# Performance work log

Hardware: AMD Instinct MI355X
Metric: run time of the kernel (lower is better)

The kernel has to match this reference:

```python
import jax, jax.numpy as jnp
import numpy as np

NUM_CLIP_VIT_FEAT = 576  # default kwarg of mixed_mask


def _mixed_mask(pad_ends, full_starts, full_ends, bt2i, blm, B, S):
    # Faithful translation of OmniAttentionMechanism.mixed_mask evaluated over
    # all (b, q_idx, kv_idx). Note python operator precedence: & binds tighter
    # than ^, so the original expression is (A&t2i) ^ (B&C&lm) ^ (D&mmu).
    q_idx = jnp.arange(S)[:, None]          # [S,1]
    kv_idx = jnp.arange(S)[None, :]         # [1,S]
    causal_qk = q_idx >= kv_idx             # [S,S]
    # kv_idx < pad_ends[b, kv_idx]  ->  arange(S) < pad_ends  (per batch row)
    pad_region = jnp.arange(S) < pad_ends   # [B,S] over kv
    causal = (~pad_region)[:, None, :] & causal_qk[None]              # [B,S,S]
    # full block: kv in [full_starts[q], full_ends[q])
    full = (kv_idx < full_ends[:, None]) & (kv_idx >= full_starts[:, None])  # [S,S]
    eye = q_idx == kv_idx                                             # [S,S]
    t2i = eye[None] ^ (causal | full[None])                           # [B,S,S]
    lm = causal_qk                                                    # [S,S]
    mmu = causal_qk | (kv_idx <= NUM_CLIP_VIT_FEAT + 3)               # [S,S]
    b = jnp.arange(B)[:, None, None]
    mask = ((b < bt2i) & t2i) \
         ^ ((b >= bt2i) & (b < bt2i + blm) & lm[None]) \
         ^ ((b >= bt2i + blm) & mmu[None])
    return mask  # [B,S,S] bool


def setup_inputs() -> dict:
    key = jax.random.key(0)
    B_T2I, B_LM, B_MMU = 4, 4, 4
    B, H, S, D = B_T2I + B_LM + B_MMU, 8, 1024, 64
    k1, k2, k3 = jax.random.split(key, 3)
    q = jax.random.normal(k1, (B, H, S, D), jnp.float32)
    k = jax.random.normal(k2, (B, H, S, D), jnp.float32)
    v = jax.random.normal(k3, (B, H, S, D), jnp.float32)

    # full_starts/full_ends from image_begin_ends=[(512,1024)]
    full_starts = np.arange(S)
    full_ends = np.arange(S)
    for ib, ie in [(512, 1024)]:
        full_starts[ib:ie] = ib
        full_ends[ib:ie] = ie

    # pad_ends from default pad_begin_ends=[(0,256),(0,300),(0,400),(0,0)]
    pad_ends = np.tile(np.arange(S), (B, 1))
    for cnt, (pb, pe) in enumerate([(0, 256), (0, 300), (0, 400), (0, 0)]):
        pad_ends[cnt, pb:pe] = pe

    return {
        "q": q, "k": k, "v": v,
        "pad_ends": jnp.asarray(pad_ends, jnp.int32),
        "full_starts": jnp.asarray(full_starts, jnp.int32),
        "full_ends": jnp.asarray(full_ends, jnp.int32),
        "batch_size_t2i": B_T2I,
        "batch_size_lm": B_LM,
    }


def reference(q, k, v, pad_ends, full_starts, full_ends, batch_size_t2i, batch_size_lm):
    B, H, S, D = q.shape
    mask = _mixed_mask(pad_ends, full_starts, full_ends,
                       batch_size_t2i, batch_size_lm, B, S)      # [B,S,S]
    scale = 1.0 / jnp.sqrt(jnp.asarray(D, q.dtype))
    scores = jnp.einsum('bhqd,bhkd->bhqk', q, k) * scale          # [B,H,S,S]
    scores = jnp.where(mask[:, None], scores, jnp.asarray(-1e30, scores.dtype))
    attn = jax.nn.softmax(scores, axis=-1)
    return jnp.einsum('bhqk,bhkd->bhqd', attn, v)
```

## Files before the change

### kernel.cpp

```cpp
#include <hip/hip_runtime.h>


typedef __attribute__((ext_vector_type(8))) short short8;
typedef __attribute__((ext_vector_type(4))) float floatx4;

#define S_LEN 1024
#define D_DIM 64
#define H_NUM 8
#define B_NUM 12
#define BT2I_CONST 4
#define BLM_CONST 4
#define NUM_CLIP_P3 579
#define KV_ELEMS (B_NUM * H_NUM * S_LEN * D_DIM)
#define P_EPS 7.888609052210118e-31f

__device__ __forceinline__ float bf2f(short s) {
    unsigned int u = ((unsigned int)(unsigned short)s) << 16;
    return __builtin_bit_cast(float, u);
}
__device__ __forceinline__ short f2bf(float f) {
    unsigned int u = __builtin_bit_cast(unsigned int, f);
    unsigned int r = (u + 0x7fffu + ((u >> 16) & 1u)) >> 16;
    return (short)(unsigned short)r;
}
__device__ __forceinline__ short scale_bf(short x) {
    float f = bf2f(x) * 0.125f;
    return (short)(unsigned short)(__builtin_bit_cast(unsigned int, f) >> 16);
}
__device__ __forceinline__ int detect_bf16(const unsigned int* q) {
    int l = threadIdx.x & 63;
    unsigned int w = q[l];
    unsigned int e = (w >> 7) & 0xffu;
    bool sane = (e >= 100u && e <= 140u);
    unsigned long long m = __ballot(sane);
    return (__popcll(m) > 32) ? 1 : 0;
}

__global__ __launch_bounds__(256)
void preprocess_kv(const void* __restrict__ Kv, const void* __restrict__ Vv,
                   const unsigned int* __restrict__ Qw,
                   short* __restrict__ Kw, short* __restrict__ Vtw) {
    __shared__ short Ls[64][66];
    const int is_bf16 = detect_bf16(Qw);
    const int x = blockIdx.x;
    const int t = threadIdx.x;
    if (x < 3072) {
        long long i0 = ((long long)x * 256 + t) * 8;
        short8 out;
        if (is_bf16) {
            out = *(const short8*)((const short*)Kv + i0);
        } else {
            const floatx4* p = (const floatx4*)((const float*)Kv + i0);
            floatx4 f0 = p[0], f1 = p[1];
            #pragma unroll
            for (int j = 0; j < 4; ++j) { out[j] = f2bf(f0[j]); out[4 + j] = f2bf(f1[j]); }
        }
        *(short8*)(Kw + i0) = out;
    } else {
        const int idx = x - 3072;
        const int tile = idx & 15, bh = idx >> 4;
        const int kvbase = tile * 64;
        const long long base = (long long)bh * S_LEN * D_DIM;
        #pragma unroll
        for (int j = 0; j < 4; ++j) {
            int lin = j * 1024 + t * 4;
            int row = lin >> 6, col = lin & 63;
            long long src = base + (long long)(kvbase + row) * D_DIM + col;
            if (is_bf16) {
                const short* p = (const short*)Vv + src;
                Ls[row][col] = p[0]; Ls[row][col + 1] = p[1];
                Ls[row][col + 2] = p[2]; Ls[row][col + 3] = p[3];
            } else {
                floatx4 f = *(const floatx4*)((const float*)Vv + src);
                Ls[row][col] = f2bf(f[0]); Ls[row][col + 1] = f2bf(f[1]);
                Ls[row][col + 2] = f2bf(f[2]); Ls[row][col + 3] = f2bf(f[3]);
            }
        }
        __syncthreads();
        const int d = t >> 2, k0 = (t & 3) * 16;
        short tmp[16];
        #pragma unroll
        for (int j = 0; j < 16; ++j) tmp[j] = Ls[k0 + j][d];
        long long dst = (long long)bh * D_DIM * S_LEN + (long long)d * S_LEN + kvbase + k0;
        *(short8*)(Vtw + dst)     = *(short8*)&tmp[0];
        *(short8*)(Vtw + dst + 8) = *(short8*)&tmp[8];
    }
}

__global__ __launch_bounds__(256, 3)
void omni_attn_main(const void* __restrict__ Qv, const int* __restrict__ pad_ends,
                    const int* __restrict__ fstarts, const int* __restrict__ fends,
                    const short* __restrict__ Kw, const short* __restrict__ Vtw,
                    float* __restrict__ Out) {
    __shared__ short Ks[64][72];
    __shared__ short Vts[64][72];
    __shared__ short Ps[4][32][72];
    __shared__ unsigned int padbits[32];

    const int lid = blockIdx.x;
    const int h = lid & 7;
    const int perm = lid >> 3;
    const int b = perm >> 3;
    const int j = perm & 7;
    const int lpt[8] = {7, 0, 6, 1, 5, 2, 4, 3};
    const int qtb = lpt[j];
    const int qb0 = qtb * 128;

    const int t = threadIdx.x;
    const int wq = t >> 6;
    const int l = t & 63;
    const int lane16 = l & 15;
    const int quad = l >> 4;

    const int is_bf16 = detect_bf16((const unsigned int*)Qv);
    const int cls = (b < BT2I_CONST) ? 0 : ((b < BT2I_CONST + BLM_CONST) ? 1 : 2);
    const int bh = b * H_NUM + h;
    const long long base = (long long)bh * S_LEN * D_DIM;

    #pragma unroll
    for (int kk = 0; kk < 4; ++kk) {
        int k = kk * 256 + t;
        bool nonpad = (k >= pad_ends[b * S_LEN + k]);
        unsigned long long m = __ballot(nonpad);
        if (l == 0) {
            int widx = kk * 8 + wq * 2;
            padbits[widx]     = (unsigned int)m;
            padbits[widx + 1] = (unsigned int)(m >> 32);
        }
    }
    __syncthreads();

    int fs_min, fe_max, fnp;
    {
        int fsv = min(fstarts[qb0 + l], fstarts[qb0 + 64 + l]);
        int fev = max(fends[qb0 + l],   fends[qb0 + 64 + l]);
        unsigned int word = 0u;
        if (l < 32) word = padbits[l];
        int pos = word ? (l * 32 + __builtin_ctz(word)) : 0x7fffffff;
        #pragma unroll
        for (int off = 1; off < 64; off <<= 1) {
            fsv = min(fsv, __shfl_xor(fsv, off, 64));
            fev = max(fev, __shfl_xor(fev, off, 64));
            pos = min(pos, __shfl_xor(pos, off, 64));
        }
        fs_min = fsv; fe_max = fev; fnp = pos;
    }
    const int qmax_blk = qb0 + 127;
    const bool risky = (cls == 0) && (fnp >= qb0) && (fnp <= qmax_blk);

    short8 aq[2][2];
    #pragma unroll
    for (int rb = 0; rb < 2; ++rb) {
        const int row = qb0 + wq * 32 + rb * 16 + lane16;
        if (is_bf16) {
            const short8* qp = (const short8*)((const short*)Qv + base
                                               + (long long)row * D_DIM + quad * 8);
            short8 r0 = qp[0], r1 = qp[4];
            #pragma unroll
            for (int jj = 0; jj < 8; ++jj) {
                aq[rb][0][jj] = scale_bf(r0[jj]);
                aq[rb][1][jj] = scale_bf(r1[jj]);
            }
        } else {
            const floatx4* qp = (const floatx4*)((const float*)Qv + base
                                                 + (long long)row * D_DIM + quad * 8);
            floatx4 f0 = qp[0], f1 = qp[1], f2 = qp[8], f3 = qp[9];
            #pragma unroll
            for (int jj = 0; jj < 4; ++jj) {
                aq[rb][0][jj]     = f2bf(f0[jj] * 0.125f);
                aq[rb][0][4 + jj] = f2bf(f1[jj] * 0.125f);
                aq[rb][1][jj]     = f2bf(f2[jj] * 0.125f);
                aq[rb][1][4 + jj] = f2bf(f3[jj] * 0.125f);
            }
        }
    }

    int qg[2][4], fs[2][4], fe[2][4];
    #pragma unroll
    for (int rb = 0; rb < 2; ++rb)
        #pragma unroll
        for (int r = 0; r < 4; ++r) {
            qg[rb][r] = qb0 + wq * 32 + rb * 16 + quad * 4 + r;
            fs[rb][r] = fstarts[qg[rb][r]];
            fe[rb][r] = fends[qg[rb][r]];
        }

    floatx4 Oc[2][4];
    float lsum[2][4];
    #pragma unroll
    for (int rb = 0; rb < 2; ++rb) {
        #pragma unroll
        for (int c = 0; c < 4; ++c) Oc[rb][c] = (floatx4){0.f, 0.f, 0.f, 0.f};
        #pragma unroll
        for (int r = 0; r < 4; ++r) lsum[rb][r] = 0.f;
    }

    const short* Kbh  = Kw  + base;
    const short* Vtbh = Vtw + (long long)bh * D_DIM * S_LEN;

    for (int kt = 0; kt < 16; ++kt) {
        const int kvbase = kt * 64;
        const unsigned int w0 = padbits[kt * 2], w1 = padbits[kt * 2 + 1];
        bool keep;
        if (cls == 0) {
            bool allpad = (w0 | w1) == 0u;
            keep = risky ||
                   ((kvbase < fe_max) && (kvbase + 64 > fs_min)) ||
                   ((kvbase <= qmax_blk) && (!allpad || (kvbase >= qb0)));
        } else if (cls == 1) {
            keep = (kvbase <= qmax_blk);
        } else {
            keep = (kvbase <= qmax_blk) || (kvbase <= NUM_CLIP_P3);
        }
        if (!keep) continue;

        __syncthreads();

        {
            const int r0 = t >> 2, s = t & 3;
            const short8* gk = (const short8*)(Kbh + (long long)(kvbase + r0) * D_DIM);
            *(short8*)&Ks[r0][s * 8]       = gk[s];
            *(short8*)&Ks[r0][(s + 4) * 8] = gk[s + 4];
            const short8* gv = (const short8*)(Vtbh + (long long)r0 * S_LEN + kvbase);
            *(short8*)&Vts[r0][s * 8]       = gv[s];
            *(short8*)&Vts[r0][(s + 4) * 8] = gv[s + 4];
        }
        __syncthreads();

        int col[4], knp[4];
        #pragma unroll
        for (int f = 0; f < 4; ++f) {
            int c16 = f * 16 + lane16;
            col[f] = kvbase + c16;
            knp[f] = (int)(((f < 2 ? w0 : w1) >> (c16 & 31)) & 1u);
        }

        #pragma unroll
        for (int rb = 0; rb < 2; ++rb) {
            floatx4 sc[4];
            #pragma unroll
            for (int f = 0; f < 4; ++f) {
                short8 b0 = *(const short8*)&Ks[f * 16 + lane16][quad * 8];
                short8 b1 = *(const short8*)&Ks[f * 16 + lane16][32 + quad * 8];
                floatx4 c = (floatx4){0.f, 0.f, 0.f, 0.f};
                c = __builtin_amdgcn_mfma_f32_16x16x32_bf16(aq[rb][0], b0, c, 0, 0, 0);
                c = __builtin_amdgcn_mfma_f32_16x16x32_bf16(aq[rb][1], b1, c, 0, 0, 0);
                sc[f] = c;
            }
            if (cls == 0) {
                #pragma unroll
                for (int r = 0; r < 4; ++r) {
                    const int q = qg[rb][r];
                    #pragma unroll
                    for (int f = 0; f < 4; ++f) {
                        const int k = col[f];
                        bool causal = knp[f] && (q >= k);
                        bool full   = (k >= fs[rb][r]) && (k < fe[rb][r]);
                        bool m      = (q == k) != (causal || full);
                        sc[f][r] = m ? sc[f][r] : -1e30f;
                    }
                }
            } else if (cls == 1) {
                #pragma unroll
                for (int r = 0; r < 4; ++r) {
                    const int q = qg[rb][r];
                    #pragma unroll
                    for (int f = 0; f < 4; ++f)
                        sc[f][r] = (q >= col[f]) ? sc[f][r] : -1e30f;
                }
            } else {
                #pragma unroll
                for (int r = 0; r < 4; ++r) {
                    const int q = qg[rb][r];
                    #pragma unroll
                    for (int f = 0; f < 4; ++f) {
                        bool m = (q >= col[f]) || (col[f] <= NUM_CLIP_P3);
                        sc[f][r] = m ? sc[f][r] : -1e30f;
                    }
                }
            }
            #pragma unroll
            for (int r = 0; r < 4; ++r) {
                #pragma unroll
                for (int f = 0; f < 4; ++f) {
                    float p = __expf(sc[f][r]) + P_EPS;
                    sc[f][r] = p;
                    lsum[rb][r] += p;
                }
            }
            #pragma unroll
            for (int r = 0; r < 4; ++r)
                #pragma unroll
                for (int f = 0; f < 4; ++f)
                    Ps[wq][rb * 16 + quad * 4 + r][f * 16 + lane16] = f2bf(sc[f][r]);
        }

        asm volatile("s_waitcnt lgkmcnt(0)" ::: "memory");

        short8 pa[2][2];
        #pragma unroll
        for (int rb = 0; rb < 2; ++rb) {
            pa[rb][0] = *(const short8*)&Ps[wq][rb * 16 + lane16][quad * 8];
            pa[rb][1] = *(const short8*)&Ps[wq][rb * 16 + lane16][32 + quad * 8];
        }
        #pragma unroll
        for (int c = 0; c < 4; ++c) {
            short8 b0 = *(const short8*)&Vts[c * 16 + lane16][quad * 8];
            short8 b1 = *(const short8*)&Vts[c * 16 + lane16][32 + quad * 8];
            Oc[0][c] = __builtin_amdgcn_mfma_f32_16x16x32_bf16(pa[0][0], b0, Oc[0][c], 0, 0, 0);
            Oc[0][c] = __builtin_amdgcn_mfma_f32_16x16x32_bf16(pa[0][1], b1, Oc[0][c], 0, 0, 0);
            Oc[1][c] = __builtin_amdgcn_mfma_f32_16x16x32_bf16(pa[1][0], b0, Oc[1][c], 0, 0, 0);
            Oc[1][c] = __builtin_amdgcn_mfma_f32_16x16x32_bf16(pa[1][1], b1, Oc[1][c], 0, 0, 0);
        }
    }

    #pragma unroll
    for (int rb = 0; rb < 2; ++rb) {
        float* ob = Out + ((long long)bh * S_LEN + qb0 + wq * 32 + rb * 16) * D_DIM;
        #pragma unroll
        for (int r = 0; r < 4; ++r) {
            float s = lsum[rb][r];
            s += __shfl_xor(s, 1, 64);
            s += __shfl_xor(s, 2, 64);
            s += __shfl_xor(s, 4, 64);
            s += __shfl_xor(s, 8, 64);
            float inv = 1.0f / s;
            #pragma unroll
            for (int c = 0; c < 4; ++c)
                ob[(quad * 4 + r) * D_DIM + c * 16 + lane16] = Oc[rb][c][r] * inv;
        }
    }
}

__global__ __launch_bounds__(256)
void omni_attn_fallback(const void* __restrict__ Qv, const void* __restrict__ Kv,
                        const void* __restrict__ Vv, const int* __restrict__ pad_ends,
                        const int* __restrict__ fstarts, const int* __restrict__ fends,
                        float* __restrict__ Out) {
    __shared__ short Ks[64][72];
    __shared__ short Vts[64][72];
    __shared__ short Ps[4][16][72];
    __shared__ int   padv[64];
    const int qt = blockIdx.x, h = blockIdx.y, b = blockIdx.z;
    const int t = threadIdx.x, wq = t >> 6, l = t & 63;
    const int lane16 = l & 15, quad = l >> 4;
    const int is_bf16 = detect_bf16((const unsigned int*)Qv);
    const int cls = (b < BT2I_CONST) ? 0 : ((b < BT2I_CONST + BLM_CONST) ? 1 : 2);
    const int bh = b * H_NUM + h;
    const long long base = (long long)bh * S_LEN * D_DIM;
    const short* Kb16 = (const short*)Kv + base;
    const short* Vb16 = (const short*)Vv + base;
    const float* Kbf = (const float*)Kv + base;
    const float* Vbf = (const float*)Vv + base;
    const int qbase = qt * 64 + wq * 16;
    short8 aq0, aq1;
    if (is_bf16) {
        const short8* qp = (const short8*)((const short*)Qv + base + (qbase + lane16) * D_DIM + quad * 8);
        short8 r0 = qp[0], r1 = qp[4];
        #pragma unroll
        for (int jj = 0; jj < 8; ++jj) { aq0[jj] = scale_bf(r0[jj]); aq1[jj] = scale_bf(r1[jj]); }
    } else {
        const floatx4* qp = (const floatx4*)((const float*)Qv + base + (qbase + lane16) * D_DIM + quad * 8);
        floatx4 f0 = qp[0], f1 = qp[1], f2 = qp[8], f3 = qp[9];
        #pragma unroll
        for (int jj = 0; jj < 4; ++jj) {
            aq0[jj] = f2bf(f0[jj] * 0.125f); aq0[4 + jj] = f2bf(f1[jj] * 0.125f);
            aq1[jj] = f2bf(f2[jj] * 0.125f); aq1[4 + jj] = f2bf(f3[jj] * 0.125f);
        }
    }
    int qg[4], fs[4], fe[4];
    #pragma unroll
    for (int r = 0; r < 4; ++r) {
        qg[r] = qbase + quad * 4 + r; fs[r] = fstarts[qg[r]]; fe[r] = fends[qg[r]];
    }
    floatx4 Oc[4];
    #pragma unroll
    for (int c = 0; c < 4; ++c) Oc[c] = (floatx4){0.f, 0.f, 0.f, 0.f};
    float m_i[4] = {-1e30f, -1e30f, -1e30f, -1e30f};
    float l_i[4] = {0.f, 0.f, 0.f, 0.f};
    for (int kt = 0; kt < S_LEN / 64; ++kt) {
        const int kvbase = kt * 64;
        __syncthreads();
        {
            const int kvr = t >> 2, seg = t & 3;
            if (is_bf16) {
                const short8* gk = (const short8*)(Kb16 + (kvbase + kvr) * D_DIM);
                *(short8*)&Ks[kvr][seg * 8] = gk[seg];
                *(short8*)&Ks[kvr][(seg + 4) * 8] = gk[seg + 4];
                const short8* gv = (const short8*)(Vb16 + (kvbase + kvr) * D_DIM);
                short8 v0 = gv[seg], v1 = gv[seg + 4];
                #pragma unroll
                for (int jj = 0; jj < 8; ++jj) {
                    Vts[seg * 8 + jj][kvr] = v0[jj];
                    Vts[32 + seg * 8 + jj][kvr] = v1[jj];
                }
            } else {
                const floatx4* gk = (const floatx4*)(Kbf + (kvbase + kvr) * D_DIM);
                floatx4 k0 = gk[seg * 2], k1 = gk[seg * 2 + 1];
                floatx4 k2 = gk[8 + seg * 2], k3 = gk[8 + seg * 2 + 1];
                #pragma unroll
                for (int jj = 0; jj < 4; ++jj) {
                    Ks[kvr][seg * 8 + jj] = f2bf(k0[jj]);
                    Ks[kvr][seg * 8 + 4 + jj] = f2bf(k1[jj]);
                    Ks[kvr][32 + seg * 8 + jj] = f2bf(k2[jj]);
                    Ks[kvr][32 + seg * 8 + 4 + jj] = f2bf(k3[jj]);
                }
                const floatx4* gv = (const floatx4*)(Vbf + (kvbase + kvr) * D_DIM);
                floatx4 v0 = gv[seg * 2], v1 = gv[seg * 2 + 1];
                floatx4 v2 = gv[8 + seg * 2], v3 = gv[8 + seg * 2 + 1];
                #pragma unroll
                for (int jj = 0; jj < 4; ++jj) {
                    Vts[seg * 8 + jj][kvr] = f2bf(v0[jj]);
                    Vts[seg * 8 + 4 + jj][kvr] = f2bf(v1[jj]);
                    Vts[32 + seg * 8 + jj][kvr] = f2bf(v2[jj]);
                    Vts[32 + seg * 8 + 4 + jj][kvr] = f2bf(v3[jj]);
                }
            }
            if (t < 64) {
                int kg = kvbase + t;
                padv[t] = (kg < pad_ends[b * S_LEN + kg]) ? 1 : 0;
            }
        }
        __syncthreads();
        floatx4 sc[4];
        #pragma unroll
        for (int f = 0; f < 4; ++f) {
            short8 b0 = *(const short8*)&Ks[f * 16 + lane16][quad * 8];
            short8 b1 = *(const short8*)&Ks[f * 16 + lane16][32 + quad * 8];
            floatx4 c = (floatx4){0.f, 0.f, 0.f, 0.f};
            c = __builtin_amdgcn_mfma_f32_16x16x32_bf16(aq0, b0, c, 0, 0, 0);
            c = __builtin_amdgcn_mfma_f32_16x16x32_bf16(aq1, b1, c, 0, 0, 0);
            sc[f] = c;
        }
        int col[4], cpad[4];
        #pragma unroll
        for (int f = 0; f < 4; ++f) {
            col[f] = kvbase + f * 16 + lane16;
            cpad[f] = padv[f * 16 + lane16];
        }
        if (cls == 0) {
            #pragma unroll
            for (int r = 0; r < 4; ++r) {
                const int q = qg[r];
                #pragma unroll
                for (int f = 0; f < 4; ++f) {
                    const int k = col[f];
                    bool causal = (!cpad[f]) && (q >= k);
                    bool full = (k >= fs[r]) && (k < fe[r]);
                    bool m = (q == k) != (causal || full);
                    sc[f][r] = m ? sc[f][r] : -1e30f;
                }
            }
        } else if (cls == 1) {
            #pragma unroll
            for (int r = 0; r < 4; ++r) {
                const int q = qg[r];
                #pragma unroll
                for (int f = 0; f < 4; ++f)
                    sc[f][r] = (q >= col[f]) ? sc[f][r] : -1e30f;
            }
        } else {
            #pragma unroll
            for (int r = 0; r < 4; ++r) {
                const int q = qg[r];
                #pragma unroll
                for (int f = 0; f < 4; ++f) {
                    bool m = (q >= col[f]) || (col[f] <= NUM_CLIP_P3);
                    sc[f][r] = m ? sc[f][r] : -1e30f;
                }
            }
        }
        #pragma unroll
        for (int r = 0; r < 4; ++r) {
            float rmax = fmaxf(fmaxf(sc[0][r], sc[1][r]), fmaxf(sc[2][r], sc[3][r]));
            #pragma unroll
            for (int off = 1; off < 16; off <<= 1)
                rmax = fmaxf(rmax, __shfl_xor(rmax, off, 64));
            float mnew = fmaxf(m_i[r], rmax);
            float alpha = __expf(m_i[r] - mnew);
            m_i[r] = mnew;
            float psum = 0.f;
            #pragma unroll
            for (int f = 0; f < 4; ++f) {
                float p = __expf(sc[f][r] - mnew);
                sc[f][r] = p; psum += p;
            }
            #pragma unroll
            for (int off = 1; off < 16; off <<= 1)
                psum += __shfl_xor(psum, off, 64);
            l_i[r] = l_i[r] * alpha + psum;
            Oc[0][r] *= alpha; Oc[1][r] *= alpha; Oc[2][r] *= alpha; Oc[3][r] *= alpha;
        }
        #pragma unroll
        for (int r = 0; r < 4; ++r)
            #pragma unroll
            for (int f = 0; f < 4; ++f)
                Ps[wq][quad * 4 + r][f * 16 + lane16] = f2bf(sc[f][r]);
        __syncthreads();
        short8 a0 = *(const short8*)&Ps[wq][lane16][quad * 8];
        short8 a1 = *(const short8*)&Ps[wq][lane16][32 + quad * 8];
        #pragma unroll
        for (int c = 0; c < 4; ++c) {
            short8 b0 = *(const short8*)&Vts[c * 16 + lane16][quad * 8];
            short8 b1 = *(const short8*)&Vts[c * 16 + lane16][32 + quad * 8];
            Oc[c] = __builtin_amdgcn_mfma_f32_16x16x32_bf16(a0, b0, Oc[c], 0, 0, 0);
            Oc[c] = __builtin_amdgcn_mfma_f32_16x16x32_bf16(a1, b1, Oc[c], 0, 0, 0);
        }
    }
    float* ob = Out + ((long long)bh * S_LEN + qbase) * D_DIM;
    #pragma unroll
    for (int r = 0; r < 4; ++r) {
        float inv = 1.0f / l_i[r];
        #pragma unroll
        for (int c = 0; c < 4; ++c)
            ob[(quad * 4 + r) * D_DIM + c * 16 + lane16] = Oc[c][r] * inv;
    }
}

extern "C" void kernel_launch(void* const* d_in, const int* in_sizes, int n_in,
                              void* d_out, int out_size, void* d_ws, size_t ws_size,
                              hipStream_t stream) {
    const void* Q = d_in[0];
    const void* K = d_in[1];
    const void* V = d_in[2];
    const int* pad_ends = (const int*)d_in[3];
    const int* fstarts  = (const int*)d_in[4];
    const int* fends    = (const int*)d_in[5];
    float* Out = (float*)d_out;

    const size_t need = 2 * (size_t)KV_ELEMS * 2;

    if (ws_size >= need) {
        short* Kw  = (short*)d_ws;
        short* Vtw = Kw + KV_ELEMS;
        preprocess_kv<<<4608, 256, 0, stream>>>(K, V, (const unsigned int*)Q, Kw, Vtw);
        omni_attn_main<<<768, 256, 0, stream>>>(Q, pad_ends, fstarts, fends,
                                                Kw, Vtw, Out);
    } else {
        dim3 grid(S_LEN / 64, H_NUM, B_NUM);
        omni_attn_fallback<<<grid, 256, 0, stream>>>(Q, K, V, pad_ends, fstarts,
                                                     fends, Out);
    }
}
```

Before: 175.4 us.

## Double-buffer K/V tiles, keep P in registers, and skip mask on interior tiles

Restructures the main attention kernel in several ways. The K/V LDS tiles are double-buffered with register prefetch over a precomputed keep-mask of tiles, so global loads overlap compute and each tile needs one barrier. The QK MFMA is transposed so that P can be packed to bf16 with v_cvt_pk and redistributed across lanes with permlane swaps instead of round-tripping through LDS. A per-tile fast path skips mask evaluation when the whole tile is known to be unmasked, and the block-to-(batch,qtile) mapping is regrouped by class with per-class ordering. Risks include higher register pressure from the prefetch registers and correctness dependence on the permlane layout.

```diff
diff --git a/kernel.cpp b/kernel.cpp
--- a/kernel.cpp
+++ b/kernel.cpp
@@ -3,6 +3,7 @@
 
 typedef __attribute__((ext_vector_type(8))) short short8;
 typedef __attribute__((ext_vector_type(4))) float floatx4;
+typedef __attribute__((ext_vector_type(4))) unsigned int uint4v;
 
 #define S_LEN 1024
 #define D_DIM 64
@@ -92,18 +93,20 @@
                     const int* __restrict__ fstarts, const int* __restrict__ fends,
                     const short* __restrict__ Kw, const short* __restrict__ Vtw,
                     float* __restrict__ Out) {
-    __shared__ short Ks[64][72];
-    __shared__ short Vts[64][72];
-    __shared__ short Ps[4][32][72];
+    __shared__ short Ks[2][64][72];
+    __shared__ short Vts[2][64][72];
     __shared__ unsigned int padbits[32];
 
     const int lid = blockIdx.x;
-    const int h = lid & 7;
-    const int perm = lid >> 3;
-    const int b = perm >> 3;
-    const int j = perm & 7;
-    const int lpt[8] = {7, 0, 6, 1, 5, 2, 4, 3};
-    const int qtb = lpt[j];
+    const int grp = lid >> 8;
+    const int u   = lid & 255;
+    const int h   = u & 7;
+    const int b   = grp * 4 + (u >> 6);
+    const int j   = (u >> 3) & 7;
+    int qtb;
+    if (grp == 0)      qtb = j;
+    else if (grp == 1) qtb = 7 - j;
+    else               qtb = (int)((0x43210567u >> (4 * j)) & 7u);
     const int qb0 = qtb * 128;
 
     const int t = threadIdx.x;
@@ -113,7 +116,7 @@
     const int quad = l >> 4;
 
     const int is_bf16 = detect_bf16((const unsigned int*)Qv);
-    const int cls = (b < BT2I_CONST) ? 0 : ((b < BT2I_CONST + BLM_CONST) ? 1 : 2);
+    const int cls = grp;
     const int bh = b * H_NUM + h;
     const long long base = (long long)bh * S_LEN * D_DIM;
 
@@ -148,56 +151,8 @@
     const int qmax_blk = qb0 + 127;
     const bool risky = (cls == 0) && (fnp >= qb0) && (fnp <= qmax_blk);
 
-    short8 aq[2][2];
-    #pragma unroll
-    for (int rb = 0; rb < 2; ++rb) {
-        const int row = qb0 + wq * 32 + rb * 16 + lane16;
-        if (is_bf16) {
-            const short8* qp = (const short8*)((const short*)Qv + base
-                                               + (long long)row * D_DIM + quad * 8);
-            short8 r0 = qp[0], r1 = qp[4];
-            #pragma unroll
-            for (int jj = 0; jj < 8; ++jj) {
-                aq[rb][0][jj] = scale_bf(r0[jj]);
-                aq[rb][1][jj] = scale_bf(r1[jj]);
-            }
-        } else {
-            const floatx4* qp = (const floatx4*)((const float*)Qv + base
-                                                 + (long long)row * D_DIM + quad * 8);
-            floatx4 f0 = qp[0], f1 = qp[1], f2 = qp[8], f3 = qp[9];
-            #pragma unroll
-            for (int jj = 0; jj < 4; ++jj) {
-                aq[rb][0][jj]     = f2bf(f0[jj] * 0.125f);
-                aq[rb][0][4 + jj] = f2bf(f1[jj] * 0.125f);
-                aq[rb][1][jj]     = f2bf(f2[jj] * 0.125f);
-                aq[rb][1][4 + jj] = f2bf(f3[jj] * 0.125f);
-            }
-        }
-    }
-
-    int qg[2][4], fs[2][4], fe[2][4];
-    #pragma unroll
-    for (int rb = 0; rb < 2; ++rb)
-        #pragma unroll
-        for (int r = 0; r < 4; ++r) {
-            qg[rb][r] = qb0 + wq * 32 + rb * 16 + quad * 4 + r;
-            fs[rb][r] = fstarts[qg[rb][r]];
-            fe[rb][r] = fends[qg[rb][r]];
-        }
-
-    floatx4 Oc[2][4];
-    float lsum[2][4];
-    #pragma unroll
-    for (int rb = 0; rb < 2; ++rb) {
-        #pragma unroll
-        for (int c = 0; c < 4; ++c) Oc[rb][c] = (floatx4){0.f, 0.f, 0.f, 0.f};
-        #pragma unroll
-        for (int r = 0; r < 4; ++r) lsum[rb][r] = 0.f;
-    }
-
-    const short* Kbh  = Kw  + base;
-    const short* Vtbh = Vtw + (long long)bh * D_DIM * S_LEN;
-
+    unsigned int keepmask = 0u;
+    #pragma unroll
     for (int kt = 0; kt < 16; ++kt) {
         const int kvbase = kt * 64;
         const unsigned int w0 = padbits[kt * 2], w1 = padbits[kt * 2 + 1];
@@ -212,119 +167,202 @@
         } else {
             keep = (kvbase <= qmax_blk) || (kvbase <= NUM_CLIP_P3);
         }
-        if (!keep) continue;
-
-        __syncthreads();
-
-        {
-            const int r0 = t >> 2, s = t & 3;
-            const short8* gk = (const short8*)(Kbh + (long long)(kvbase + r0) * D_DIM);
-            *(short8*)&Ks[r0][s * 8]       = gk[s];
-            *(short8*)&Ks[r0][(s + 4) * 8] = gk[s + 4];
-            const short8* gv = (const short8*)(Vtbh + (long long)r0 * S_LEN + kvbase);
-            *(short8*)&Vts[r0][s * 8]       = gv[s];
-            *(short8*)&Vts[r0][(s + 4) * 8] = gv[s + 4];
-        }
-        __syncthreads();
-
-        int col[4], knp[4];
+        keepmask |= (keep ? 1u : 0u) << kt;
+    }
+
+    short8 aq[2][2];
+    #pragma unroll
+    for (int rb = 0; rb < 2; ++rb) {
+        const int row = qb0 + wq * 32 + rb * 16 + lane16;
+        if (is_bf16) {
+            const short8* qp = (const short8*)((const short*)Qv + base
+                                               + (long long)row * D_DIM + quad * 8);
+            short8 r0 = qp[0], r1 = qp[4];
+            #pragma unroll
+            for (int jj = 0; jj < 8; ++jj) {
+                aq[rb][0][jj] = scale_bf(r0[jj]);
+                aq[rb][1][jj] = scale_bf(r1[jj]);
+            }
+        } else {
+            const floatx4* qp = (const floatx4*)((const float*)Qv + base
+                                                 + (long long)row * D_DIM + quad * 8);
+            floatx4 f0 = qp[0], f1 = qp[1], f2 = qp[8], f3 = qp[9];
+            #pragma unroll
+            for (int jj = 0; jj < 4; ++jj) {
+                aq[rb][0][jj]     = f2bf(f0[jj] * 0.125f);
+                aq[rb][0][4 + jj] = f2bf(f1[jj] * 0.125f);
+                aq[rb][1][jj]     = f2bf(f2[jj] * 0.125f);
+                aq[rb][1][4 + jj] = f2bf(f3[jj] * 0.125f);
+            }
+        }
+    }
+
+    int qvl[2], fsl[2], fel[2], fsmax[2], femin[2];
+    #pragma unroll
+    for (int rb = 0; rb < 2; ++rb) {
+        qvl[rb] = qb0 + wq * 32 + rb * 16 + lane16;
+        fsl[rb] = fstarts[qvl[rb]];
+        fel[rb] = fends[qvl[rb]];
+        int a = fsl[rb], e = fel[rb];
+        #pragma unroll
+        for (int off = 1; off < 16; off <<= 1) {
+            a = max(a, __shfl_xor(a, off, 64));
+            e = min(e, __shfl_xor(e, off, 64));
+        }
+        fsmax[rb] = a; femin[rb] = e;
+    }
+
+    floatx4 Oc[2][4];
+    float lsum[2] = {0.f, 0.f};
+    #pragma unroll
+    for (int rb = 0; rb < 2; ++rb)
+        #pragma unroll
+        for (int c = 0; c < 4; ++c) Oc[rb][c] = (floatx4){0.f, 0.f, 0.f, 0.f};
+
+    const short* Kbh  = Kw  + base;
+    const short* Vtbh = Vtw + (long long)bh * D_DIM * S_LEN;
+    const int r0 = t >> 2, sseg = t & 3;
+
+    short8 rk0, rk1, rv0, rv1;
+    auto load_tile = [&](int kvbase) {
+        const short8* gk = (const short8*)(Kbh + (long long)(kvbase + r0) * D_DIM);
+        rk0 = gk[sseg]; rk1 = gk[sseg + 4];
+        const short8* gv = (const short8*)(Vtbh + (long long)r0 * S_LEN + kvbase);
+        rv0 = gv[sseg]; rv1 = gv[sseg + 4];
+    };
+    auto write_tile = [&](int buf) {
+        *(short8*)&Ks[buf][r0][sseg * 8]        = rk0;
+        *(short8*)&Ks[buf][r0][(sseg + 4) * 8]  = rk1;
+        *(short8*)&Vts[buf][r0][sseg * 8]       = rv0;
+        *(short8*)&Vts[buf][r0][(sseg + 4) * 8] = rv1;
+    };
+
+    auto compute_tile = [&](int kt, int buf) {
+        const int kvbase = kt * 64;
+        const unsigned int w0c = padbits[kt * 2], w1c = padbits[kt * 2 + 1];
+
+        floatx4 sc[2][4];
         #pragma unroll
         for (int f = 0; f < 4; ++f) {
-            int c16 = f * 16 + lane16;
-            col[f] = kvbase + c16;
-            knp[f] = (int)(((f < 2 ? w0 : w1) >> (c16 & 31)) & 1u);
-        }
-
+            short8 kb0 = *(const short8*)&Ks[buf][f * 16 + lane16][quad * 8];
+            short8 kb1 = *(const short8*)&Ks[buf][f * 16 + lane16][32 + quad * 8];
+            #pragma unroll
+            for (int rb = 0; rb < 2; ++rb) {
+                floatx4 c = (floatx4){0.f, 0.f, 0.f, 0.f};
+                c = __builtin_amdgcn_mfma_f32_16x16x32_bf16(kb0, aq[rb][0], c, 0, 0, 0);
+                c = __builtin_amdgcn_mfma_f32_16x16x32_bf16(kb1, aq[rb][1], c, 0, 0, 0);
+                sc[rb][f] = c;
+            }
+        }
+
+        short8 pa[2][2];
         #pragma unroll
         for (int rb = 0; rb < 2; ++rb) {
-            floatx4 sc[4];
-            #pragma unroll
-            for (int f = 0; f < 4; ++f) {
-                short8 b0 = *(const short8*)&Ks[f * 16 + lane16][quad * 8];
-                short8 b1 = *(const short8*)&Ks[f * 16 + lane16][32 + quad * 8];
-                floatx4 c = (floatx4){0.f, 0.f, 0.f, 0.f};
-                c = __builtin_amdgcn_mfma_f32_16x16x32_bf16(aq[rb][0], b0, c, 0, 0, 0);
-                c = __builtin_amdgcn_mfma_f32_16x16x32_bf16(aq[rb][1], b1, c, 0, 0, 0);
-                sc[f] = c;
-            }
+            const int qlo = qb0 + wq * 32 + rb * 16;
+            bool fast;
             if (cls == 0) {
-                #pragma unroll
-                for (int r = 0; r < 4; ++r) {
-                    const int q = qg[rb][r];
+                bool np_all  = ((w0c & w1c) == 0xffffffffu);
+                bool below   = (kvbase + 63 < qlo);
+                bool eyefree = below || (kvbase > qlo + 15);
+                fast = (np_all && below) ||
+                       (eyefree && (kvbase >= fsmax[rb]) && (kvbase + 64 <= femin[rb]));
+            } else if (cls == 1) {
+                fast = (kvbase + 63 <= qlo);
+            } else {
+                fast = (kvbase + 63 <= qlo) || (kvbase + 63 <= NUM_CLIP_P3);
+            }
+            if (!fast) {
+                const int q = qvl[rb];
+                #pragma unroll
+                for (int f = 0; f < 4; ++f) {
+                    const unsigned int word = (f < 2) ? w0c : w1c;
+                    const int sh = 16 * (f & 1) + 4 * quad;
                     #pragma unroll
-                    for (int f = 0; f < 4; ++f) {
-                        const int k = col[f];
-                        bool causal = knp[f] && (q >= k);
-                        bool full   = (k >= fs[rb][r]) && (k < fe[rb][r]);
-                        bool m      = (q == k) != (causal || full);
-                        sc[f][r] = m ? sc[f][r] : -1e30f;
+                    for (int r = 0; r < 4; ++r) {
+                        const int k = kvbase + f * 16 + 4 * quad + r;
+                        bool m;
+                        if (cls == 0) {
+                            bool knp    = ((word >> (sh + r)) & 1u) != 0u;
+                            bool causal = knp && (q >= k);
+                            bool full   = (k >= fsl[rb]) && (k < fel[rb]);
+                            m = (q == k) != (causal || full);
+                        } else if (cls == 1) {
+                            m = (q >= k);
+                        } else {
+                            m = (q >= k) || (k <= NUM_CLIP_P3);
+                        }
+                        sc[rb][f][r] = m ? sc[rb][f][r] : -1e30f;
                     }
                 }
-            } else if (cls == 1) {
-                #pragma unroll
-                for (int r = 0; r < 4; ++r) {
-                    const int q = qg[rb][r];
-                    #pragma unroll
-                    for (int f = 0; f < 4; ++f)
-                        sc[f][r] = (q >= col[f]) ? sc[f][r] : -1e30f;
-                }
-            } else {
-                #pragma unroll
-                for (int r = 0; r < 4; ++r) {
-                    const int q = qg[rb][r];
-                    #pragma unroll
-                    for (int f = 0; f < 4; ++f) {
-                        bool m = (q >= col[f]) || (col[f] <= NUM_CLIP_P3);
-                        sc[f][r] = m ? sc[f][r] : -1e30f;
-                    }
-                }
-            }
-            #pragma unroll
-            for (int r = 0; r < 4; ++r) {
-                #pragma unroll
-                for (int f = 0; f < 4; ++f) {
-                    float p = __expf(sc[f][r]) + P_EPS;
-                    sc[f][r] = p;
-                    lsum[rb][r] += p;
-                }
-            }
-            #pragma unroll
-            for (int r = 0; r < 4; ++r)
-                #pragma unroll
-                for (int f = 0; f < 4; ++f)
-                    Ps[wq][rb * 16 + quad * 4 + r][f * 16 + lane16] = f2bf(sc[f][r]);
-        }
-
-        asm volatile("s_waitcnt lgkmcnt(0)" ::: "memory");
-
-        short8 pa[2][2];
-        #pragma unroll
-        for (int rb = 0; rb < 2; ++rb) {
-            pa[rb][0] = *(const short8*)&Ps[wq][rb * 16 + lane16][quad * 8];
-            pa[rb][1] = *(const short8*)&Ps[wq][rb * 16 + lane16][32 + quad * 8];
-        }
+            }
+            unsigned int uu[4][2];
+            float ls = 0.f;
+            #pragma unroll
+            for (int f = 0; f < 4; ++f) {
+                float p0 = __expf(sc[rb][f][0]) + P_EPS;
+                float p1 = __expf(sc[rb][f][1]) + P_EPS;
+                float p2 = __expf(sc[rb][f][2]) + P_EPS;
+                float p3 = __expf(sc[rb][f][3]) + P_EPS;
+                ls += p0 + p1 + p2 + p3;
+                asm("v_cvt_pk_bf16_f32 %0, %1, %2" : "=v"(uu[f][0]) : "v"(p0), "v"(p1));
+                asm("v_cvt_pk_bf16_f32 %0, %1, %2" : "=v"(uu[f][1]) : "v"(p2), "v"(p3));
+            }
+            lsum[rb] += ls;
+            #pragma unroll
+            for (int hh = 0; hh < 2; ++hh) {
+                unsigned int x0 = uu[2 * hh][0],     y0 = uu[2 * hh + 1][0];
+                unsigned int x1 = uu[2 * hh][1],     y1 = uu[2 * hh + 1][1];
+                asm("v_permlane32_swap_b32 %0, %1" : "+v"(x0), "+v"(y0));
+                asm("v_permlane16_swap_b32 %0, %1" : "+v"(x0), "+v"(y0));
+                asm("v_permlane32_swap_b32 %0, %1" : "+v"(x1), "+v"(y1));
+                asm("v_permlane16_swap_b32 %0, %1" : "+v"(x1), "+v"(y1));
+                uint4v w;
+                w[0] = x0; w[1] = x1; w[2] = y0; w[3] = y1;
+                pa[rb][hh] = __builtin_bit_cast(short8, w);
+            }
+        }
+
         #pragma unroll
         for (int c = 0; c < 4; ++c) {
-            short8 b0 = *(const short8*)&Vts[c * 16 + lane16][quad * 8];
-            short8 b1 = *(const short8*)&Vts[c * 16 + lane16][32 + quad * 8];
-            Oc[0][c] = __builtin_amdgcn_mfma_f32_16x16x32_bf16(pa[0][0], b0, Oc[0][c], 0, 0, 0);
-            Oc[0][c] = __builtin_amdgcn_mfma_f32_16x16x32_bf16(pa[0][1], b1, Oc[0][c], 0, 0, 0);
-            Oc[1][c] = __builtin_amdgcn_mfma_f32_16x16x32_bf16(pa[1][0], b0, Oc[1][c], 0, 0, 0);
-            Oc[1][c] = __builtin_amdgcn_mfma_f32_16x16x32_bf16(pa[1][1], b1, Oc[1][c], 0, 0, 0);
-        }
+            short8 vb0 = *(const short8*)&Vts[buf][c * 16 + lane16][quad * 8];
+            short8 vb1 = *(const short8*)&Vts[buf][c * 16 + lane16][32 + quad * 8];
+            Oc[0][c] = __builtin_amdgcn_mfma_f32_16x16x32_bf16(pa[0][0], vb0, Oc[0][c], 0, 0, 0);
+            Oc[0][c] = __builtin_amdgcn_mfma_f32_16x16x32_bf16(pa[0][1], vb1, Oc[0][c], 0, 0, 0);
+            Oc[1][c] = __builtin_amdgcn_mfma_f32_16x16x32_bf16(pa[1][0], vb0, Oc[1][c], 0, 0, 0);
+            Oc[1][c] = __builtin_amdgcn_mfma_f32_16x16x32_bf16(pa[1][1], vb1, Oc[1][c], 0, 0, 0);
+        }
+    };
+
+    unsigned int mrem = keepmask;
+    int ktA = __builtin_ctz(mrem); mrem &= mrem - 1;
+    load_tile(ktA * 64);
+    int ktB = -1;
+    if (mrem) { ktB = __builtin_ctz(mrem); mrem &= mrem - 1; }
+    write_tile(0);
+    if (ktB >= 0) load_tile(ktB * 64);
+    __syncthreads();
+    int cur = 0;
+    for (;;) {
+        compute_tile(ktA, cur);
+        if (ktB < 0) break;
+        int ktC = -1;
+        if (mrem) { ktC = __builtin_ctz(mrem); mrem &= mrem - 1; }
+        write_tile(cur ^ 1);
+        if (ktC >= 0) load_tile(ktC * 64);
+        __syncthreads();
+        cur ^= 1; ktA = ktB; ktB = ktC;
     }
 
     #pragma unroll
     for (int rb = 0; rb < 2; ++rb) {
+        float s = lsum[rb];
+        s += __shfl_xor(s, 16, 64);
+        s += __shfl_xor(s, 32, 64);
         float* ob = Out + ((long long)bh * S_LEN + qb0 + wq * 32 + rb * 16) * D_DIM;
         #pragma unroll
         for (int r = 0; r < 4; ++r) {
-            float s = lsum[rb][r];
-            s += __shfl_xor(s, 1, 64);
-            s += __shfl_xor(s, 2, 64);
-            s += __shfl_xor(s, 4, 64);
-            s += __shfl_xor(s, 8, 64);
-            float inv = 1.0f / s;
+            float sv = __shfl(s, quad * 4 + r, 64);
+            float inv = 1.0f / sv;
             #pragma unroll
             for (int c = 0; c < 4; ++c)
                 ob[(quad * 4 + r) * D_DIM + c * 16 + lane16] = Oc[rb][c][r] * inv;
```

After: 197.9 us. 1.13x slower.
